# Performance work log

Hardware: AMD Instinct MI355X
Metric: run time of the kernel (lower is better)

## Reference

```python
import jax, jax.numpy as jnp
import numpy as np
from jax import lax

S, V, E, H, T = 2048, 50257, 512, 1024, 12
HD = H // 2  # per-direction hidden
START, END = 0, 1
NEG = -1e6


def setup_inputs() -> dict:
    key = jax.random.key(0)
    ks = jax.random.split(key, 16)
    sentence = jax.random.randint(ks[0], (S,), 0, V)
    gold_tags = jax.random.randint(ks[1], (S,), 2, T)  # avoid START/END gold labels
    emb = jax.random.normal(ks[2], (V, E), jnp.float32) * 0.1
    s = 0.05
    wih_f = jax.random.normal(ks[3], (4 * HD, E), jnp.float32) * s
    whh_f = jax.random.normal(ks[4], (4 * HD, HD), jnp.float32) * s
    b_f = jax.random.normal(ks[5], (4 * HD,), jnp.float32) * s
    wih_b = jax.random.normal(ks[6], (4 * HD, E), jnp.float32) * s
    whh_b = jax.random.normal(ks[7], (4 * HD, HD), jnp.float32) * s
    b_b = jax.random.normal(ks[8], (4 * HD,), jnp.float32) * s
    w_out = jax.random.normal(ks[9], (T, H), jnp.float32) * s
    b_out = jax.random.normal(ks[10], (T,), jnp.float32) * s
    transitions = jax.random.normal(ks[11], (T, T), jnp.float32)
    transitions = transitions.at[START, :].set(NEG).at[:, END].set(NEG)
    h0 = jax.random.normal(ks[12], (2, HD), jnp.float32)
    c0 = jax.random.normal(ks[13], (2, HD), jnp.float32)
    return dict(sentence=sentence, gold_tags=gold_tags, emb=emb,
                wih_f=wih_f, whh_f=whh_f, b_f=b_f,
                wih_b=wih_b, whh_b=whh_b, b_b=b_b,
                w_out=w_out, b_out=b_out, transitions=transitions,
                h0=h0, c0=c0)


def _lstm_dir(x, h0, c0, wih, whh, b):
    # x: [S, E] -> hidden states [S, HD]; PyTorch gate order i,f,g,o
    def step(carry, xt):
        h, c = carry
        g = xt @ wih.T + h @ whh.T + b
        i, f, gg, o = jnp.split(g, 4)
        i, f, o = jax.nn.sigmoid(i), jax.nn.sigmoid(f), jax.nn.sigmoid(o)
        c = f * c + i * jnp.tanh(gg)
        h = o * jnp.tanh(c)
        return (h, c), h
    _, hs = lax.scan(step, (h0, c0), x)
    return hs


def _feats(sentence, emb, wih_f, whh_f, b_f, wih_b, whh_b, b_b, w_out, b_out, h0, c0):
    x = emb[sentence]                                  # [S, E]
    hf = _lstm_dir(x, h0[0], c0[0], wih_f, whh_f, b_f)  # [S, HD]
    hb = _lstm_dir(x[::-1], h0[1], c0[1], wih_b, whh_b, b_b)[::-1]
    return jnp.concatenate([hf, hb], axis=1) @ w_out.T + b_out  # [S, T]


def _crf_nll(feats, gold_tags, transitions):
    # forward algorithm (log partition)
    init = jnp.full((T,), NEG, feats.dtype).at[START].set(0.0)
    def step(prev, feat):
        nxt = jax.nn.logsumexp(prev[None, :] + transitions + feat[:, None], axis=1)
        return nxt, None
    final, _ = lax.scan(step, init, feats)
    alpha = jax.nn.logsumexp(final + transitions[END])
    # gold score
    tags = jnp.concatenate([jnp.array([START], gold_tags.dtype), gold_tags])
    trans_score = jnp.sum(transitions[tags[1:], tags[:-1]])
    emit_score = jnp.sum(feats[jnp.arange(feats.shape[0]), tags[1:]])
    gold = trans_score + emit_score + transitions[END, tags[-1]]
    return alpha - gold


def reference(sentence, gold_tags, emb, wih_f, whh_f, b_f, wih_b, whh_b, b_b,
              w_out, b_out, transitions, h0, c0):
    feats = _feats(sentence, emb, wih_f, whh_f, b_f, wih_b, whh_b, b_b,
                   w_out, b_out, h0, c0)
    return _crf_nll(feats, gold_tags, transitions)
```

## Files before the change

### kernel.cpp

```cpp
#include <hip/hip_runtime.h>

#define S 2048
#define HD 512
#define EDIM 512
#define NT 12
#define G4 2048
#define NWGD 16
#define JPW 32
#define RPW 128
#define HSTR 36

typedef unsigned short ushort_t;
typedef unsigned int uint_t;

__device__ __forceinline__ ushort_t f2b(float f) {
    uint_t u = __float_as_uint(f);
    uint_t r = u + 0x7fffu + ((u >> 16) & 1u);
    return (ushort_t)(r >> 16);
}
__device__ __forceinline__ float b2f(ushort_t h) {
    return __uint_as_float(((uint_t)h) << 16);
}
__device__ __forceinline__ float sigm(float x) { return 1.f / (1.f + __expf(-x)); }
__device__ __forceinline__ float tanh_(float x) {
    float e = __expf(2.f * x);
    return 1.f - 2.f / (e + 1.f);
}

__global__ __launch_bounds__(256, 2)
void xw_gemm(const int* __restrict__ sentence, const float* __restrict__ emb,
             const float* __restrict__ wih_f, const float* __restrict__ b_f,
             const float* __restrict__ wih_b, const float* __restrict__ b_b,
             ushort_t* __restrict__ xw) {
    __shared__ float As[32][68];
    __shared__ float Bs[32][68];
    __shared__ int toks[64];
    const int tid = threadIdx.x;
    const int tbase = blockIdx.x * 64;
    const int rbase = blockIdx.y * 64;
    const int dir = blockIdx.z;
    const float* wih = dir ? wih_b : wih_f;
    const float* bia = dir ? b_b : b_f;
    if (tid < 64) {
        int tt = tbase + tid;
        toks[tid] = sentence[dir ? (S - 1 - tt) : tt];
    }
    __syncthreads();
    const int lm = tid >> 2;
    const int lk = (tid & 3) * 8;
    const int ty = tid >> 4, tx = tid & 15;
    const float* aBase = emb + (size_t)toks[lm] * EDIM + lk;
    const float* bBase = wih + (size_t)(rbase + lm) * EDIM + lk;
    float acc[4][4];
#pragma unroll
    for (int i = 0; i < 4; ++i)
#pragma unroll
        for (int j = 0; j < 4; ++j) acc[i][j] = 0.f;

    for (int kc = 0; kc < EDIM; kc += 32) {
        float4 a0 = ((const float4*)(aBase + kc))[0];
        float4 a1 = ((const float4*)(aBase + kc))[1];
        float4 b0 = ((const float4*)(bBase + kc))[0];
        float4 b1 = ((const float4*)(bBase + kc))[1];
        __syncthreads();
        As[lk + 0][lm] = a0.x; As[lk + 1][lm] = a0.y; As[lk + 2][lm] = a0.z; As[lk + 3][lm] = a0.w;
        As[lk + 4][lm] = a1.x; As[lk + 5][lm] = a1.y; As[lk + 6][lm] = a1.z; As[lk + 7][lm] = a1.w;
        Bs[lk + 0][lm] = b0.x; Bs[lk + 1][lm] = b0.y; Bs[lk + 2][lm] = b0.z; Bs[lk + 3][lm] = b0.w;
        Bs[lk + 4][lm] = b1.x; Bs[lk + 5][lm] = b1.y; Bs[lk + 6][lm] = b1.z; Bs[lk + 7][lm] = b1.w;
        __syncthreads();
#pragma unroll
        for (int kk = 0; kk < 32; ++kk) {
            float4 a4 = *(const float4*)&As[kk][ty * 4];
            float4 b4 = *(const float4*)&Bs[kk][tx * 4];
            float av[4] = {a4.x, a4.y, a4.z, a4.w};
            float bv[4] = {b4.x, b4.y, b4.z, b4.w};
#pragma unroll
            for (int i = 0; i < 4; ++i)
#pragma unroll
                for (int j = 0; j < 4; ++j) acc[i][j] = fmaf(av[i], bv[j], acc[i][j]);
        }
    }
    float4 bi = *(const float4*)&bia[rbase + tx * 4];
    float bvv[4] = {bi.x, bi.y, bi.z, bi.w};
#pragma unroll
    for (int i = 0; i < 4; ++i) {
        ushort4 o;
        o.x = f2b(acc[i][0] + bvv[0]);
        o.y = f2b(acc[i][1] + bvv[1]);
        o.z = f2b(acc[i][2] + bvv[2]);
        o.w = f2b(acc[i][3] + bvv[3]);
        ushort_t* p = xw + ((size_t)dir * S + tbase + ty * 4 + i) * G4 + rbase + tx * 4;
        *(ushort4*)p = o;
    }
}

__global__ __launch_bounds__(512, 1)
void lstm_rec(const float* __restrict__ whh_f, const float* __restrict__ whh_b,
              const float* __restrict__ h0, const float* __restrict__ c0,
              const ushort_t* __restrict__ xw, float* hs) {
    __shared__ float hstage[16 * HSTR];
    __shared__ float gates[RPW];
    const int tid = threadIdx.x;
    const int dir = blockIdx.x >> 4;
    const int wg = blockIdx.x & 15;
    const int jbase = wg * JPW;
    const int rg = tid >> 4, kc = tid & 15;
    const float* whh = dir ? whh_b : whh_f;

    const int r0 = rg * 4;
    const int g = r0 >> 5;
    const int u0 = r0 & 31;
    const size_t xwrow = (size_t)g * HD + jbase + u0;

    float4 w[4][8];
#pragma unroll
    for (int ri = 0; ri < 4; ++ri) {
        const float* wrow = whh + (size_t)(g * HD + jbase + u0 + ri) * HD + kc * 32;
#pragma unroll
        for (int i = 0; i < 8; ++i) w[ri][i] = *(const float4*)(wrow + i * 4);
    }

    const ushort_t* xwd = xw + (size_t)dir * S * G4;
    float* hsd = hs + (size_t)dir * S * HD;

    float cj = 0.f;
    if (tid < JPW) cj = c0[dir * HD + jbase + tid];

    if (tid < 256) {
        int c = tid >> 4, m = (2 * tid) & 31;
        hstage[c * HSTR + m] = h0[dir * HD + 2 * tid];
        hstage[c * HSTR + m + 1] = h0[dir * HD + 2 * tid + 1];
    }
    __syncthreads();

    const bool isw = (kc == 0);
    for (int t = 0; t < S; ++t) {
        float xv[4] = {0.f, 0.f, 0.f, 0.f};
        if (isw) {
            ushort4 x4 = *(const ushort4*)&xwd[(size_t)t * G4 + xwrow];
            xv[0] = b2f(x4.x); xv[1] = b2f(x4.y); xv[2] = b2f(x4.z); xv[3] = b2f(x4.w);
        }
        float a0 = 0.f, a1 = 0.f, a2 = 0.f, a3 = 0.f;
#pragma unroll
        for (int i = 0; i < 8; ++i) {
            float4 h4 = *(const float4*)&hstage[kc * HSTR + i * 4];
            a0 = fmaf(w[0][i].x, h4.x, a0); a0 = fmaf(w[0][i].y, h4.y, a0);
            a0 = fmaf(w[0][i].z, h4.z, a0); a0 = fmaf(w[0][i].w, h4.w, a0);
            a1 = fmaf(w[1][i].x, h4.x, a1); a1 = fmaf(w[1][i].y, h4.y, a1);
            a1 = fmaf(w[1][i].z, h4.z, a1); a1 = fmaf(w[1][i].w, h4.w, a1);
            a2 = fmaf(w[2][i].x, h4.x, a2); a2 = fmaf(w[2][i].y, h4.y, a2);
            a2 = fmaf(w[2][i].z, h4.z, a2); a2 = fmaf(w[2][i].w, h4.w, a2);
            a3 = fmaf(w[3][i].x, h4.x, a3); a3 = fmaf(w[3][i].y, h4.y, a3);
            a3 = fmaf(w[3][i].z, h4.z, a3); a3 = fmaf(w[3][i].w, h4.w, a3);
        }
#pragma unroll
        for (int m = 1; m < 16; m <<= 1) {
            a0 += __shfl_xor(a0, m); a1 += __shfl_xor(a1, m);
            a2 += __shfl_xor(a2, m); a3 += __shfl_xor(a3, m);
        }
        if (isw) {
            gates[r0 + 0] = a0 + xv[0];
            gates[r0 + 1] = a1 + xv[1];
            gates[r0 + 2] = a2 + xv[2];
            gates[r0 + 3] = a3 + xv[3];
        }
        __syncthreads();
        if (tid < JPW) {
            float ai = gates[tid], af = gates[JPW + tid];
            float ag = gates[2 * JPW + tid], ao = gates[3 * JPW + tid];
            float ii = sigm(ai), ff = sigm(af), gg = tanh_(ag), oo = sigm(ao);
            cj = ff * cj + ii * gg;
            float hnew = oo * tanh_(cj);
            __hip_atomic_store(&hsd[(size_t)t * HD + jbase + tid], hnew,
                               __ATOMIC_RELAXED, __HIP_MEMORY_SCOPE_AGENT);
        }
        if (t < S - 1 && tid < 256) {
            const unsigned long long* p0 =
                (const unsigned long long*)&hsd[(size_t)t * HD + 2 * tid];
            float v0, v1;
            for (;;) {
                unsigned long long v =
                    __hip_atomic_load(p0, __ATOMIC_RELAXED, __HIP_MEMORY_SCOPE_AGENT);
                uint_t lo = (uint_t)v, hi = (uint_t)(v >> 32);
                if (lo != 0xFFFFFFFFu && hi != 0xFFFFFFFFu) {
                    v0 = __uint_as_float(lo);
                    v1 = __uint_as_float(hi);
                    break;
                }
            }
            int c = tid >> 4, m = (2 * tid) & 31;
            hstage[c * HSTR + m] = v0;
            hstage[c * HSTR + m + 1] = v1;
        }
        __syncthreads();
    }
}

__global__ __launch_bounds__(256)
void feats_k(const float* __restrict__ hs, const float* __restrict__ w_out,
             const float* __restrict__ b_out, float* __restrict__ feats) {
    const int t = blockIdx.x, tid = threadIdx.x;
    float4 h4;
    if (tid < 128)
        h4 = *(const float4*)&hs[(size_t)t * HD + tid * 4];
    else
        h4 = *(const float4*)&hs[(size_t)S * HD + (size_t)(S - 1 - t) * HD + (tid - 128) * 4];
    float acc[NT];
#pragma unroll
    for (int tg = 0; tg < NT; ++tg) {
        float4 w4 = *(const float4*)&w_out[(size_t)tg * 1024 + tid * 4];
        acc[tg] = h4.x * w4.x + h4.y * w4.y + h4.z * w4.z + h4.w * w4.w;
    }
#pragma unroll
    for (int m = 1; m < 64; m <<= 1)
#pragma unroll
        for (int tg = 0; tg < NT; ++tg) acc[tg] += __shfl_xor(acc[tg], m);
    __shared__ float part[4][NT];
    if ((tid & 63) == 0) {
#pragma unroll
        for (int tg = 0; tg < NT; ++tg) part[tid >> 6][tg] = acc[tg];
    }
    __syncthreads();
    if (tid < NT)
        feats[(size_t)t * NT + tid] =
            part[0][tid] + part[1][tid] + part[2][tid] + part[3][tid] + b_out[tid];
}

__global__ __launch_bounds__(256, 1)
void crf_k(const float* __restrict__ feats, const int* __restrict__ gold,
           const float* __restrict__ trans, float* __restrict__ out) {
    extern __shared__ float sfeats[];
    __shared__ float red[256];
    __shared__ float nprev[NT];
    __shared__ float tr[144];
    __shared__ float gold_sh;
    const int tid = threadIdx.x;
    for (int i = tid; i < S * NT / 4; i += 256)
        ((float4*)sfeats)[i] = ((const float4*)feats)[i];
    if (tid < 144) tr[tid] = trans[tid];
    __syncthreads();
    float gsum = 0.f;
    for (int t = tid; t < S; t += 256) {
        int a = gold[t];
        int b = t ? gold[t - 1] : 0;
        gsum += tr[a * NT + b] + sfeats[t * NT + a];
    }
    red[tid] = gsum;
    __syncthreads();
    for (int s = 128; s; s >>= 1) {
        if (tid < s) red[tid] += red[tid + s];
        __syncthreads();
    }
    if (tid == 0) gold_sh = red[0] + tr[1 * NT + gold[S - 1]];
    __syncthreads();
    const int i = tid >> 4, j = tid & 15;
    const bool act = (tid < 192) && (j < NT);
    float tij = act ? tr[i * NT + j] : -3e38f;
    float prev = (j == 0) ? 0.f : -1e6f;
    for (int t = 0; t < S; ++t) {
        float v = act ? (prev + tij) : -3e38f;
        float mx = v;
        mx = fmaxf(mx, __shfl_xor(mx, 1));
        mx = fmaxf(mx, __shfl_xor(mx, 2));
        mx = fmaxf(mx, __shfl_xor(mx, 4));
        mx = fmaxf(mx, __shfl_xor(mx, 8));
        float e = __expf(v - mx);
        float ss = e;
        ss += __shfl_xor(ss, 1);
        ss += __shfl_xor(ss, 2);
        ss += __shfl_xor(ss, 4);
        ss += __shfl_xor(ss, 8);
        if (tid < 192 && j == 0) nprev[i] = mx + __logf(ss) + sfeats[t * NT + i];
        __syncthreads();
        prev = nprev[j < NT ? j : 0];
        __syncthreads();
    }
    if (tid < 64) {
        float v2 = (tid < NT) ? prev + tr[1 * NT + tid] : -3e38f;
        float mx = v2;
        mx = fmaxf(mx, __shfl_xor(mx, 1));
        mx = fmaxf(mx, __shfl_xor(mx, 2));
        mx = fmaxf(mx, __shfl_xor(mx, 4));
        mx = fmaxf(mx, __shfl_xor(mx, 8));
        float e = __expf(v2 - mx);
        float ss = e;
        ss += __shfl_xor(ss, 1);
        ss += __shfl_xor(ss, 2);
        ss += __shfl_xor(ss, 4);
        ss += __shfl_xor(ss, 8);
        if (tid == 0) out[0] = (mx + __logf(ss)) - gold_sh;
    }
}

extern "C" void kernel_launch(void* const* d_in, const int* in_sizes, int n_in,
                              void* d_out, int out_size, void* d_ws, size_t ws_size,
                              hipStream_t stream) {
    const int* sentence = (const int*)d_in[0];
    const int* gold = (const int*)d_in[1];
    const float* emb = (const float*)d_in[2];
    const float* wih_f = (const float*)d_in[3];
    const float* whh_f = (const float*)d_in[4];
    const float* b_f = (const float*)d_in[5];
    const float* wih_b = (const float*)d_in[6];
    const float* whh_b = (const float*)d_in[7];
    const float* b_b = (const float*)d_in[8];
    const float* w_out = (const float*)d_in[9];
    const float* b_out = (const float*)d_in[10];
    const float* trans = (const float*)d_in[11];
    const float* h0 = (const float*)d_in[12];
    const float* c0 = (const float*)d_in[13];
    float* out = (float*)d_out;

    char* ws = (char*)d_ws;
    const size_t XW_B = (size_t)2 * S * G4 * 2;
    const size_t HS_B = (size_t)2 * S * HD * 4;
    ushort_t* xw = (ushort_t*)ws;
    float* hs = (float*)(ws + XW_B);
    float* feats = (float*)(ws + XW_B + HS_B);

    hipMemsetAsync(hs, 0xFF, HS_B, stream);

    dim3 gg(S / 64, G4 / 64, 2);
    xw_gemm<<<gg, 256, 0, stream>>>(sentence, emb, wih_f, b_f, wih_b, b_b, xw);

    lstm_rec<<<2 * NWGD, 512, 0, stream>>>(whh_f, whh_b, h0, c0, xw, hs);

    feats_k<<<S, 256, 0, stream>>>(hs, w_out, b_out, feats);

    const size_t CRF_LDS = (size_t)S * NT * 4;
    hipFuncSetAttribute((const void*)crf_k,
                        hipFuncAttributeMaxDynamicSharedMemorySize, (int)CRF_LDS);
    crf_k<<<1, 256, CRF_LDS, stream>>>(feats, gold, trans, out);
}
```

Measured before the change: 5.247 ms.

## Remap LSTM rows so each lane owns all four gates, drop a barrier

```diff
diff --git a/kernel.cpp b/kernel.cpp
--- a/kernel.cpp
+++ b/kernel.cpp
@@ -7,7 +7,6 @@
 #define G4 2048
 #define NWGD 16
 #define JPW 32
-#define RPW 128
 #define HSTR 36
 
 typedef unsigned short ushort_t;
@@ -98,52 +97,59 @@
 void lstm_rec(const float* __restrict__ whh_f, const float* __restrict__ whh_b,
               const float* __restrict__ h0, const float* __restrict__ c0,
               const ushort_t* __restrict__ xw, float* hs) {
-    __shared__ float hstage[16 * HSTR];
-    __shared__ float gates[RPW];
+    __shared__ float hstage[2][16 * HSTR];
     const int tid = threadIdx.x;
     const int dir = blockIdx.x >> 4;
     const int wg = blockIdx.x & 15;
     const int jbase = wg * JPW;
     const int rg = tid >> 4, kc = tid & 15;
     const float* whh = dir ? whh_b : whh_f;
-
-    const int r0 = rg * 4;
-    const int g = r0 >> 5;
-    const int u0 = r0 & 31;
-    const size_t xwrow = (size_t)g * HD + jbase + u0;
+    const int u = jbase + rg;
 
     float4 w[4][8];
 #pragma unroll
-    for (int ri = 0; ri < 4; ++ri) {
-        const float* wrow = whh + (size_t)(g * HD + jbase + u0 + ri) * HD + kc * 32;
-#pragma unroll
-        for (int i = 0; i < 8; ++i) w[ri][i] = *(const float4*)(wrow + i * 4);
+    for (int g = 0; g < 4; ++g) {
+        const float* wrow = whh + (size_t)(g * HD + u) * HD + kc * 32;
+#pragma unroll
+        for (int i = 0; i < 8; ++i) w[g][i] = *(const float4*)(wrow + i * 4);
     }
 
     const ushort_t* xwd = xw + (size_t)dir * S * G4;
     float* hsd = hs + (size_t)dir * S * HD;
 
+    const bool isw = (kc == 0);
     float cj = 0.f;
-    if (tid < JPW) cj = c0[dir * HD + jbase + tid];
+    if (isw) cj = c0[dir * HD + u];
 
     if (tid < 256) {
         int c = tid >> 4, m = (2 * tid) & 31;
-        hstage[c * HSTR + m] = h0[dir * HD + 2 * tid];
-        hstage[c * HSTR + m + 1] = h0[dir * HD + 2 * tid + 1];
-    }
-    __syncthreads();
-
-    const bool isw = (kc == 0);
+        hstage[0][c * HSTR + m] = h0[dir * HD + 2 * tid];
+        hstage[0][c * HSTR + m + 1] = h0[dir * HD + 2 * tid + 1];
+    }
+    __syncthreads();
+
+    ushort_t xr[4] = {0, 0, 0, 0};
+    if (isw) {
+#pragma unroll
+        for (int g = 0; g < 4; ++g) xr[g] = xwd[(size_t)g * HD + u];
+    }
+
     for (int t = 0; t < S; ++t) {
-        float xv[4] = {0.f, 0.f, 0.f, 0.f};
-        if (isw) {
-            ushort4 x4 = *(const ushort4*)&xwd[(size_t)t * G4 + xwrow];
-            xv[0] = b2f(x4.x); xv[1] = b2f(x4.y); xv[2] = b2f(x4.z); xv[3] = b2f(x4.w);
-        }
+        const int pb = t & 1;
+        const float* hb = hstage[pb];
+        float* hw = hstage[pb ^ 1];
+
+        ushort_t xn[4] = {0, 0, 0, 0};
+        if (isw && t + 1 < S) {
+#pragma unroll
+            for (int g = 0; g < 4; ++g)
+                xn[g] = xwd[(size_t)(t + 1) * G4 + g * HD + u];
+        }
+
         float a0 = 0.f, a1 = 0.f, a2 = 0.f, a3 = 0.f;
 #pragma unroll
         for (int i = 0; i < 8; ++i) {
-            float4 h4 = *(const float4*)&hstage[kc * HSTR + i * 4];
+            float4 h4 = *(const float4*)&hb[kc * HSTR + i * 4];
             a0 = fmaf(w[0][i].x, h4.x, a0); a0 = fmaf(w[0][i].y, h4.y, a0);
             a0 = fmaf(w[0][i].z, h4.z, a0); a0 = fmaf(w[0][i].w, h4.w, a0);
             a1 = fmaf(w[1][i].x, h4.x, a1); a1 = fmaf(w[1][i].y, h4.y, a1);
@@ -159,38 +165,29 @@
             a2 += __shfl_xor(a2, m); a3 += __shfl_xor(a3, m);
         }
         if (isw) {
-            gates[r0 + 0] = a0 + xv[0];
-            gates[r0 + 1] = a1 + xv[1];
-            gates[r0 + 2] = a2 + xv[2];
-            gates[r0 + 3] = a3 + xv[3];
-        }
-        __syncthreads();
-        if (tid < JPW) {
-            float ai = gates[tid], af = gates[JPW + tid];
-            float ag = gates[2 * JPW + tid], ao = gates[3 * JPW + tid];
-            float ii = sigm(ai), ff = sigm(af), gg = tanh_(ag), oo = sigm(ao);
+            float ii = sigm(a0 + b2f(xr[0]));
+            float ff = sigm(a1 + b2f(xr[1]));
+            float gg = tanh_(a2 + b2f(xr[2]));
+            float oo = sigm(a3 + b2f(xr[3]));
             cj = ff * cj + ii * gg;
             float hnew = oo * tanh_(cj);
-            __hip_atomic_store(&hsd[(size_t)t * HD + jbase + tid], hnew,
+            __hip_atomic_store(&hsd[(size_t)t * HD + u], hnew,
                                __ATOMIC_RELAXED, __HIP_MEMORY_SCOPE_AGENT);
+            xr[0] = xn[0]; xr[1] = xn[1]; xr[2] = xn[2]; xr[3] = xn[3];
         }
         if (t < S - 1 && tid < 256) {
             const unsigned long long* p0 =
                 (const unsigned long long*)&hsd[(size_t)t * HD + 2 * tid];
-            float v0, v1;
+            uint_t lo, hi;
             for (;;) {
                 unsigned long long v =
                     __hip_atomic_load(p0, __ATOMIC_RELAXED, __HIP_MEMORY_SCOPE_AGENT);
-                uint_t lo = (uint_t)v, hi = (uint_t)(v >> 32);
-                if (lo != 0xFFFFFFFFu && hi != 0xFFFFFFFFu) {
-                    v0 = __uint_as_float(lo);
-                    v1 = __uint_as_float(hi);
-                    break;
-                }
+                lo = (uint_t)v; hi = (uint_t)(v >> 32);
+                if (lo != 0xFFFFFFFFu && hi != 0xFFFFFFFFu) break;
             }
             int c = tid >> 4, m = (2 * tid) & 31;
-            hstage[c * HSTR + m] = v0;
-            hstage[c * HSTR + m + 1] = v1;
+            hw[c * HSTR + m] = __uint_as_float(lo);
+            hw[c * HSTR + m + 1] = __uint_as_float(hi);
         }
         __syncthreads();
     }
```

Measured after the change: 6.192 ms. 18.0% more time.
